# Kernel tuning notes

Measured on AMD Instinct MI355X. Metric: run time of the kernel, lower is better.

The kernel has to match this reference:

```python
import jax, jax.numpy as jnp
import numpy as np

IN_F, OUT_F, RANK, ALPHA, NUM_ADAPTERS = 1024, 1024, 8, 1.0, 8
B, S = 32, 1024
SCALE = ALPHA / RANK


def setup_inputs() -> dict:
    key = jax.random.key(0)
    k1, k2, k3, k4, k5, k6 = jax.random.split(key, 6)
    x = jax.random.normal(k1, (B, S, IN_F), dtype=jnp.float32)
    subject_id = jax.random.randint(k2, (B,), 0, NUM_ADAPTERS)
    # base linear: W [out,in], bias [out] (torch nn.Linear layout)
    W = jax.random.normal(k3, (OUT_F, IN_F), dtype=jnp.float32) * (1.0 / np.sqrt(IN_F))
    b = jax.random.normal(k4, (OUT_F,), dtype=jnp.float32) * 0.01
    # stacked LoRA weights: A [E, rank, in], Bw [E, out, rank]
    # (original inits Bw to zeros; randomized here so the LoRA path is exercised)
    A = jax.random.normal(k5, (NUM_ADAPTERS, RANK, IN_F), dtype=jnp.float32) * 0.02
    Bw = jax.random.normal(k6, (NUM_ADAPTERS, OUT_F, RANK), dtype=jnp.float32) * 0.02
    return {"x": x, "W": W, "b": b, "A": A, "Bw": Bw, "subject_id": subject_id}


def reference(x, W, b, A, Bw, subject_id):
    # base linear: [B,S,O]
    out = jnp.einsum("bsd,od->bso", x, W) + b
    # gather per-batch adapter weights (equivalent to the per-adapter mask loop)
    A_sel = A[subject_id]   # [B, rank, in]
    B_sel = Bw[subject_id]  # [B, out, rank]
    h = jnp.einsum("bsd,brd->bsr", x, A_sel)          # [B,S,rank]
    lora = jnp.einsum("bsr,bor->bso", h, B_sel) * SCALE  # [B,S,out]
    return out + lora
```

## Files before the change

### kernel.cpp

```cpp
#include <hip/hip_runtime.h>
#include <hip/hip_bf16.h>

typedef __bf16 bf16_t;
typedef bf16_t bf16x4 __attribute__((ext_vector_type(4)));
typedef bf16_t bf16x8 __attribute__((ext_vector_type(8)));
typedef float  f32x4  __attribute__((ext_vector_type(4)));

#define IN_F   1024
#define OUT_F  1024
#define RANK   8
#define NE     8
#define BATCH  32
#define SEQ    1024
#define M_TOT  (BATCH * SEQ)
#define SCALE  0.125f
#define NT     16

#define GLOAD_LDS16(g, l)                                                     \
  __builtin_amdgcn_global_load_lds(                                           \
      (const __attribute__((address_space(1))) void*)(g),                     \
      (__attribute__((address_space(3))) void*)(l), 16, 0, 0)

#define CFENCE asm volatile("" ::: "memory")
#define BAR()                                                                 \
  do { CFENCE; __builtin_amdgcn_s_barrier(); CFENCE; } while (0)
#define VMCNT(n) asm volatile("s_waitcnt vmcnt(" #n ")" ::: "memory")

__global__ __launch_bounds__(256) void build_weff(
    const float* __restrict__ W, const float* __restrict__ A,
    const float* __restrict__ Bw, bf16_t* __restrict__ weff) {
  const int e  = blockIdx.x >> 10;
  const int o  = blockIdx.x & 1023;
  const int d0 = threadIdx.x << 2;

  f32x4 acc = *(const f32x4*)(W + ((size_t)o << 10) + d0);
  const float* bwr = Bw + (((size_t)e << 10) + o) * RANK;
  const float* ab  = A + (((size_t)e * RANK) << 10) + d0;
#pragma unroll
  for (int r = 0; r < RANK; ++r) {
    const float s = SCALE * bwr[r];
    const f32x4 a4 = *(const f32x4*)(ab + ((size_t)r << 10));
    acc += s * a4;
  }
  bf16x4 ov;
#pragma unroll
  for (int j = 0; j < 4; ++j) ov[j] = (bf16_t)acc[j];
  *(bf16x4*)(weff + (((size_t)e << 10) + o) * IN_F + d0) = ov;
}

__global__ __launch_bounds__(256) void cvt_x(const float* __restrict__ x,
                                             bf16_t* __restrict__ xb, int n4) {
  int i = blockIdx.x * 256 + threadIdx.x;
  const int stride = gridDim.x * 256;
  for (; i < n4; i += stride) {
    const f32x4 v = *(const f32x4*)(x + ((size_t)i << 2));
    bf16x4 o;
#pragma unroll
    for (int j = 0; j < 4; ++j) o[j] = (bf16_t)v[j];
    *(bf16x4*)(xb + ((size_t)i << 2)) = o;
  }
}

__global__ __launch_bounds__(512, 2) void gemm256(
    const bf16_t* __restrict__ xb, const bf16_t* __restrict__ weff,
    const float* __restrict__ bias, const int* __restrict__ sid,
    float* __restrict__ out) {
  __shared__ bf16_t lds[2][2][2][8192];

  const int bid0 = blockIdx.x;
  const int wgid = ((bid0 & 7) << 6) + (bid0 >> 3);
  const int mb = wgid >> 2, nb = wgid & 3;
  const int m0 = mb << 8, n0 = nb << 8;
  const int e = sid[mb >> 2];

  const int tid = threadIdx.x;
  const int lane = tid & 63, wid = tid >> 6;
  const int wm = wid >> 2, wn = wid & 3;

  const bf16_t* agbase = xb + ((size_t)m0 << 10);
  const bf16_t* bgbase = weff + ((size_t)e << 20) + ((size_t)n0 << 10);

  int soff[2];
#pragma unroll
  for (int i = 0; i < 2; ++i) {
    const int r = (wid << 5) + (i << 4) + (lane >> 2);
    const int sg = (lane & 3) ^ ((r >> 1) & 3);
    soff[i] = (r << 10) + (sg << 3);
  }

  int aoff[8], boff[4];
#pragma unroll
  for (int mi = 0; mi < 8; ++mi) {
    const int r = (wm << 7) + (mi << 4) + (lane & 15);
    const int g = (lane >> 4) ^ ((r >> 1) & 3);
    aoff[mi] = (r << 5) + (g << 3);
  }
#pragma unroll
  for (int ni = 0; ni < 4; ++ni) {
    const int r = (wn << 6) + (ni << 4) + (lane & 15);
    const int g = (lane >> 4) ^ ((r >> 1) & 3);
    boff[ni] = (r << 5) + (g << 3);
  }

  f32x4 acc[8][4] = {};

#define STAGE(gbase, mat, kt, kh)                                             \
  do {                                                                        \
    bf16_t* _d = &lds[(kt) & 1][mat][kh][wid << 10];                          \
    const int _kc = ((kt) << 6) + ((kh) << 5);                                \
    GLOAD_LDS16((gbase) + _kc + soff[0], _d);                                 \
    GLOAD_LDS16((gbase) + _kc + soff[1], _d + 512);                           \
  } while (0)

#define PHASE_READS(kt, kh)                                                   \
  do {                                                                        \
    const bf16_t* _ab = &lds[(kt) & 1][0][kh][0];                             \
    const bf16_t* _bb = &lds[(kt) & 1][1][kh][0];                             \
    _Pragma("unroll") for (int mi = 0; mi < 8; ++mi)                          \
        af[mi] = *(const bf16x8*)(_ab + aoff[mi]);                            \
    _Pragma("unroll") for (int ni = 0; ni < 4; ++ni)                          \
        bfr[ni] = *(const bf16x8*)(_bb + boff[ni]);                           \
  } while (0)

#define MFMAS()                                                               \
  do {                                                                        \
    __builtin_amdgcn_s_setprio(1);                                            \
    _Pragma("unroll") for (int mi = 0; mi < 8; ++mi)                          \
        _Pragma("unroll") for (int ni = 0; ni < 4; ++ni)                      \
            acc[mi][ni] = __builtin_amdgcn_mfma_f32_16x16x32_bf16(            \
                af[mi], bfr[ni], acc[mi][ni], 0, 0, 0);                       \
    __builtin_amdgcn_s_setprio(0);                                            \
  } while (0)

  STAGE(agbase, 0, 0, 0); STAGE(bgbase, 1, 0, 0);
  STAGE(agbase, 0, 0, 1); STAGE(bgbase, 1, 0, 1);
  STAGE(agbase, 0, 1, 0); STAGE(bgbase, 1, 1, 0);
  VMCNT(4);
  BAR();

  bf16x8 af[8], bfr[4];
  for (int j = 0; j < NT - 2; ++j) {
    PHASE_READS(j, 0);
    STAGE(agbase, 0, j + 1, 1); STAGE(bgbase, 1, j + 1, 1);
    BAR();
    MFMAS();
    BAR();
    PHASE_READS(j, 1);
    STAGE(agbase, 0, j + 2, 0); STAGE(bgbase, 1, j + 2, 0);
    VMCNT(4);
    BAR();
    MFMAS();
    BAR();
  }
  PHASE_READS(NT - 2, 0);
  STAGE(agbase, 0, NT - 1, 1); STAGE(bgbase, 1, NT - 1, 1);
  BAR();
  MFMAS();
  BAR();
  PHASE_READS(NT - 2, 1);
  VMCNT(0);
  BAR();
  MFMAS();
  BAR();
  PHASE_READS(NT - 1, 0);
  MFMAS();
  PHASE_READS(NT - 1, 1);
  MFMAS();

  const int R0 = m0 + (wm << 7);
  const int C0 = n0 + (wn << 6);
  const int crow = (lane >> 4) << 2;
  const int ccol = lane & 15;
#pragma unroll
  for (int ni = 0; ni < 4; ++ni) {
    const int col = C0 + (ni << 4) + ccol;
    const float bv = bias[col];
#pragma unroll
    for (int mi = 0; mi < 8; ++mi) {
      const int row = R0 + (mi << 4) + crow;
#pragma unroll
      for (int j2 = 0; j2 < 4; ++j2)
        out[((size_t)(row + j2) << 10) + col] = acc[mi][ni][j2] + bv;
    }
  }
#undef STAGE
#undef PHASE_READS
#undef MFMAS
}

__global__ __launch_bounds__(256) void lora_naive(
    const float* __restrict__ x, const float* __restrict__ W,
    const float* __restrict__ bias, const float* __restrict__ A,
    const float* __restrict__ Bw, const int* __restrict__ sid,
    float* __restrict__ out) {
  const int m = blockIdx.x;
  const int e = sid[m >> 10];
  __shared__ float xs[IN_F];
  __shared__ float h[RANK];
  const int tid = threadIdx.x;
  for (int i = tid; i < IN_F; i += 256) xs[i] = x[((size_t)m << 10) + i];
  __syncthreads();
  if (tid < RANK) {
    float s = 0.f;
    const float* ar = A + (((size_t)e * RANK + tid) << 10);
    for (int d = 0; d < IN_F; ++d) s += xs[d] * ar[d];
    h[tid] = s * SCALE;
  }
  __syncthreads();
  for (int o = tid; o < OUT_F; o += 256) {
    const float* wr = W + ((size_t)o << 10);
    float s = 0.f;
    for (int d = 0; d < IN_F; ++d) s += xs[d] * wr[d];
    const float* bwr = Bw + (((size_t)e << 10) + o) * RANK;
    float l = 0.f;
#pragma unroll
    for (int r = 0; r < RANK; ++r) l += h[r] * bwr[r];
    out[((size_t)m << 10) + o] = s + bias[o] + l;
  }
}

extern "C" void kernel_launch(void* const* d_in, const int* in_sizes, int n_in,
                              void* d_out, int out_size, void* d_ws,
                              size_t ws_size, hipStream_t stream) {
  const float* x   = (const float*)d_in[0];
  const float* W   = (const float*)d_in[1];
  const float* b   = (const float*)d_in[2];
  const float* A   = (const float*)d_in[3];
  const float* Bw  = (const float*)d_in[4];
  const int*   sid = (const int*)d_in[5];
  float* out = (float*)d_out;

  const size_t weff_bytes = (size_t)NE * OUT_F * IN_F * 2;
  const size_t xb_bytes   = (size_t)M_TOT * IN_F * 2;

  if (ws_size >= weff_bytes + xb_bytes) {
    bf16_t* weff = (bf16_t*)d_ws;
    bf16_t* xb   = (bf16_t*)((char*)d_ws + weff_bytes);
    hipLaunchKernelGGL(build_weff, dim3(NE * OUT_F), dim3(256), 0, stream,
                       W, A, Bw, weff);
    hipLaunchKernelGGL(cvt_x, dim3(4096), dim3(256), 0, stream,
                       x, xb, M_TOT * IN_F / 4);
    hipLaunchKernelGGL(gemm256, dim3((M_TOT / 256) * (OUT_F / 256)),
                       dim3(512), 0, stream, xb, weff, b, sid, out);
  } else {
    hipLaunchKernelGGL(lora_naive, dim3(M_TOT), dim3(256), 0, stream,
                       x, W, b, A, Bw, sid, out);
  }
}
```

Before: 139.3 us.

## Fuse fp32-to-bf16 conversion of x into the GEMM A-tile staging

Removes the separate cvt_x kernel and its bf16 workspace copy of x. The GEMM now loads fp32 x tiles into registers, converts them to bf16, and writes them into swizzled LDS, prefetching one k-tile ahead. B tiles keep using direct global-to-LDS loads. This avoids a full extra read/write pass over the activations, at the cost of doubled A-tile global bytes per GEMM block, extra registers and VALU conversion, and added lgkm waits.

```diff
diff --git a/kernel.cpp b/kernel.cpp
--- a/kernel.cpp
+++ b/kernel.cpp
@@ -25,6 +25,7 @@
 #define BAR()                                                                 \
   do { CFENCE; __builtin_amdgcn_s_barrier(); CFENCE; } while (0)
 #define VMCNT(n) asm volatile("s_waitcnt vmcnt(" #n ")" ::: "memory")
+#define LGKM0()  asm volatile("s_waitcnt lgkmcnt(0)" ::: "memory")
 
 __global__ __launch_bounds__(256) void build_weff(
     const float* __restrict__ W, const float* __restrict__ A,
@@ -48,21 +49,8 @@
   *(bf16x4*)(weff + (((size_t)e << 10) + o) * IN_F + d0) = ov;
 }
 
-__global__ __launch_bounds__(256) void cvt_x(const float* __restrict__ x,
-                                             bf16_t* __restrict__ xb, int n4) {
-  int i = blockIdx.x * 256 + threadIdx.x;
-  const int stride = gridDim.x * 256;
-  for (; i < n4; i += stride) {
-    const f32x4 v = *(const f32x4*)(x + ((size_t)i << 2));
-    bf16x4 o;
-#pragma unroll
-    for (int j = 0; j < 4; ++j) o[j] = (bf16_t)v[j];
-    *(bf16x4*)(xb + ((size_t)i << 2)) = o;
-  }
-}
-
-__global__ __launch_bounds__(512, 2) void gemm256(
-    const bf16_t* __restrict__ xb, const bf16_t* __restrict__ weff,
+__global__ __launch_bounds__(512, 2) void gemm_fused(
+    const float* __restrict__ xf, const bf16_t* __restrict__ weff,
     const float* __restrict__ bias, const int* __restrict__ sid,
     float* __restrict__ out) {
   __shared__ bf16_t lds[2][2][2][8192];
@@ -77,7 +65,7 @@
   const int lane = tid & 63, wid = tid >> 6;
   const int wm = wid >> 2, wn = wid & 3;
 
-  const bf16_t* agbase = xb + ((size_t)m0 << 10);
+  const float*  agf   = xf + ((size_t)m0 << 10);
   const bf16_t* bgbase = weff + ((size_t)e << 20) + ((size_t)n0 << 10);
 
   int soff[2];
@@ -88,6 +76,20 @@
     soff[i] = (r << 10) + (sg << 3);
   }
 
+  int agoff[4], awoff[4];
+  {
+    const int c0 = (tid & 7) << 3;
+    const int kh = c0 >> 5;
+    const int cg = (c0 >> 3) & 3;
+#pragma unroll
+    for (int q = 0; q < 4; ++q) {
+      const int r = (q << 6) + (tid >> 3);
+      agoff[q] = (r << 10) + c0;
+      const int gs = cg ^ ((r >> 1) & 3);
+      awoff[q] = (kh << 13) + (r << 5) + (gs << 3);
+    }
+  }
+
   int aoff[8], boff[4];
 #pragma unroll
   for (int mi = 0; mi < 8; ++mi) {
@@ -103,13 +105,36 @@
   }
 
   f32x4 acc[8][4] = {};
-
-#define STAGE(gbase, mat, kt, kh)                                             \
-  do {                                                                        \
-    bf16_t* _d = &lds[(kt) & 1][mat][kh][wid << 10];                          \
+  f32x4 ar[8];
+
+#define A_ISSUE(kt)                                                           \
+  do {                                                                        \
+    const float* _x = agf + ((kt) << 6);                                      \
+    _Pragma("unroll") for (int q = 0; q < 4; ++q) {                           \
+      ar[2 * q]     = *(const f32x4*)(_x + agoff[q]);                         \
+      ar[2 * q + 1] = *(const f32x4*)(_x + agoff[q] + 4);                     \
+    }                                                                         \
+  } while (0)
+
+#define A_WRITE(kt)                                                           \
+  do {                                                                        \
+    bf16_t* _ab = &lds[(kt) & 1][0][0][0];                                    \
+    _Pragma("unroll") for (int q = 0; q < 4; ++q) {                           \
+      bf16x8 v;                                                               \
+      _Pragma("unroll") for (int i2 = 0; i2 < 4; ++i2) {                      \
+        v[i2]     = (bf16_t)ar[2 * q][i2];                                    \
+        v[4 + i2] = (bf16_t)ar[2 * q + 1][i2];                                \
+      }                                                                       \
+      *(bf16x8*)(_ab + awoff[q]) = v;                                         \
+    }                                                                         \
+  } while (0)
+
+#define BSTAGE(kt, kh)                                                        \
+  do {                                                                        \
+    bf16_t* _d = &lds[(kt) & 1][1][kh][wid << 10];                            \
     const int _kc = ((kt) << 6) + ((kh) << 5);                                \
-    GLOAD_LDS16((gbase) + _kc + soff[0], _d);                                 \
-    GLOAD_LDS16((gbase) + _kc + soff[1], _d + 512);                           \
+    GLOAD_LDS16(bgbase + _kc + soff[0], _d);                                  \
+    GLOAD_LDS16(bgbase + _kc + soff[1], _d + 512);                            \
   } while (0)
 
 #define PHASE_READS(kt, kh)                                                   \
@@ -132,33 +157,41 @@
     __builtin_amdgcn_s_setprio(0);                                            \
   } while (0)
 
-  STAGE(agbase, 0, 0, 0); STAGE(bgbase, 1, 0, 0);
-  STAGE(agbase, 0, 0, 1); STAGE(bgbase, 1, 0, 1);
-  STAGE(agbase, 0, 1, 0); STAGE(bgbase, 1, 1, 0);
-  VMCNT(4);
+  A_ISSUE(0);
+  BSTAGE(0, 0); BSTAGE(0, 1);
+  A_WRITE(0);
+  A_ISSUE(1);
+  BSTAGE(1, 0);
+  VMCNT(10);
+  LGKM0();
   BAR();
 
   bf16x8 af[8], bfr[4];
   for (int j = 0; j < NT - 2; ++j) {
     PHASE_READS(j, 0);
-    STAGE(agbase, 0, j + 1, 1); STAGE(bgbase, 1, j + 1, 1);
+    A_WRITE(j + 1);
+    A_ISSUE(j + 2);
+    BSTAGE(j + 1, 1);
     BAR();
     MFMAS();
     BAR();
     PHASE_READS(j, 1);
-    STAGE(agbase, 0, j + 2, 0); STAGE(bgbase, 1, j + 2, 0);
-    VMCNT(4);
+    BSTAGE(j + 2, 0);
+    VMCNT(2);
+    LGKM0();
     BAR();
     MFMAS();
     BAR();
   }
   PHASE_READS(NT - 2, 0);
-  STAGE(agbase, 0, NT - 1, 1); STAGE(bgbase, 1, NT - 1, 1);
+  A_WRITE(NT - 1);
+  BSTAGE(NT - 1, 1);
   BAR();
   MFMAS();
   BAR();
   PHASE_READS(NT - 2, 1);
   VMCNT(0);
+  LGKM0();
   BAR();
   MFMAS();
   BAR();
@@ -183,7 +216,9 @@
         out[((size_t)(row + j2) << 10) + col] = acc[mi][ni][j2] + bv;
     }
   }
-#undef STAGE
+#undef A_ISSUE
+#undef A_WRITE
+#undef BSTAGE
 #undef PHASE_READS
 #undef MFMAS
 }
@@ -231,17 +266,13 @@
   float* out = (float*)d_out;
 
   const size_t weff_bytes = (size_t)NE * OUT_F * IN_F * 2;
-  const size_t xb_bytes   = (size_t)M_TOT * IN_F * 2;
-
-  if (ws_size >= weff_bytes + xb_bytes) {
+
+  if (ws_size >= weff_bytes) {
     bf16_t* weff = (bf16_t*)d_ws;
-    bf16_t* xb   = (bf16_t*)((char*)d_ws + weff_bytes);
     hipLaunchKernelGGL(build_weff, dim3(NE * OUT_F), dim3(256), 0, stream,
                        W, A, Bw, weff);
-    hipLaunchKernelGGL(cvt_x, dim3(4096), dim3(256), 0, stream,
-                       x, xb, M_TOT * IN_F / 4);
-    hipLaunchKernelGGL(gemm256, dim3((M_TOT / 256) * (OUT_F / 256)),
-                       dim3(512), 0, stream, xb, weff, b, sid, out);
+    hipLaunchKernelGGL(gemm_fused, dim3((M_TOT / 256) * (OUT_F / 256)),
+                       dim3(512), 0, stream, x, weff, b, sid, out);
   } else {
     hipLaunchKernelGGL(lora_naive, dim3(M_TOT), dim3(256), 0, stream,
                        x, W, b, A, Bw, sid, out);
```

New measurement: 119.8 us. 14.0% less time.

## Restructure GEMM LDS pipeline to one barrier per half-tile, nontemporal output stores

Applied to the files above, without the earlier changes.

Reworks the double-buffered global-to-LDS pipeline so each half-k phase does one vmcnt wait plus one barrier before its LDS reads, then issues the next tile's loads into the other buffer and runs the MFMAs. This removes the second barrier per phase and the separate peeled tail iterations. It keeps roughly one half-tile of prefetch in flight instead of the earlier deeper staging, which could expose more load latency. Output stores now use nontemporal hints to avoid polluting cache with the large fp32 result.

```diff
diff --git a/kernel.cpp b/kernel.cpp
--- a/kernel.cpp
+++ b/kernel.cpp
@@ -104,12 +104,15 @@
 
   f32x4 acc[8][4] = {};
 
-#define STAGE(gbase, mat, kt, kh)                                             \
+#define STAGE2(kt, kh)                                                        \
   do {                                                                        \
-    bf16_t* _d = &lds[(kt) & 1][mat][kh][wid << 10];                          \
+    bf16_t* _da = &lds[(kt) & 1][0][kh][wid << 10];                           \
+    bf16_t* _db = &lds[(kt) & 1][1][kh][wid << 10];                           \
     const int _kc = ((kt) << 6) + ((kh) << 5);                                \
-    GLOAD_LDS16((gbase) + _kc + soff[0], _d);                                 \
-    GLOAD_LDS16((gbase) + _kc + soff[1], _d + 512);                           \
+    GLOAD_LDS16(agbase + _kc + soff[0], _da);                                 \
+    GLOAD_LDS16(agbase + _kc + soff[1], _da + 512);                           \
+    GLOAD_LDS16(bgbase + _kc + soff[0], _db);                                 \
+    GLOAD_LDS16(bgbase + _kc + soff[1], _db + 512);                           \
   } while (0)
 
 #define PHASE_READS(kt, kh)                                                   \
@@ -132,38 +135,28 @@
     __builtin_amdgcn_s_setprio(0);                                            \
   } while (0)
 
-  STAGE(agbase, 0, 0, 0); STAGE(bgbase, 1, 0, 0);
-  STAGE(agbase, 0, 0, 1); STAGE(bgbase, 1, 0, 1);
-  STAGE(agbase, 0, 1, 0); STAGE(bgbase, 1, 1, 0);
-  VMCNT(4);
-  BAR();
+  STAGE2(0, 0);
+  STAGE2(0, 1);
 
   bf16x8 af[8], bfr[4];
-  for (int j = 0; j < NT - 2; ++j) {
+  for (int j = 0; j < NT - 1; ++j) {
+    VMCNT(4);
+    BAR();
     PHASE_READS(j, 0);
-    STAGE(agbase, 0, j + 1, 1); STAGE(bgbase, 1, j + 1, 1);
-    BAR();
+    STAGE2(j + 1, 0);
     MFMAS();
+    VMCNT(4);
     BAR();
     PHASE_READS(j, 1);
-    STAGE(agbase, 0, j + 2, 0); STAGE(bgbase, 1, j + 2, 0);
-    VMCNT(4);
-    BAR();
+    STAGE2(j + 1, 1);
     MFMAS();
-    BAR();
-  }
-  PHASE_READS(NT - 2, 0);
-  STAGE(agbase, 0, NT - 1, 1); STAGE(bgbase, 1, NT - 1, 1);
-  BAR();
-  MFMAS();
-  BAR();
-  PHASE_READS(NT - 2, 1);
-  VMCNT(0);
-  BAR();
-  MFMAS();
+  }
+  VMCNT(4);
   BAR();
   PHASE_READS(NT - 1, 0);
   MFMAS();
+  VMCNT(0);
+  BAR();
   PHASE_READS(NT - 1, 1);
   MFMAS();
 
@@ -180,10 +173,11 @@
       const int row = R0 + (mi << 4) + crow;
 #pragma unroll
       for (int j2 = 0; j2 < 4; ++j2)
-        out[((size_t)(row + j2) << 10) + col] = acc[mi][ni][j2] + bv;
+        __builtin_nontemporal_store(acc[mi][ni][j2] + bv,
+                                    &out[((size_t)(row + j2) << 10) + col]);
     }
   }
-#undef STAGE
+#undef STAGE2
 #undef PHASE_READS
 #undef MFMAS
 }
```

Result: faster. 128.3 us (-7.9%).
